# Performance work log

Measured on AMD Instinct MI355X. Metric: run time of the kernel, lower is better.

The kernel has to match this reference:

```python
import jax, jax.numpy as jnp
import numpy as np

B, T, P, H = 64, 64, 32, 256  # batch, seq_len, num_series, hidden


def setup_inputs() -> dict:
    key = jax.random.key(0)
    ks = jax.random.split(key, 16)
    s = 0.05  # weight init scale (keeps gates unsaturated, like PyTorch's 1/sqrt(H) init)
    return {
        'X': jax.random.normal(ks[0], (B, T, P), dtype=jnp.float32),
        'eps': jax.random.normal(ks[1], (1, B, H), dtype=jnp.float32),
        'W_ih_enc': jax.random.normal(ks[2], (3 * H, P), dtype=jnp.float32) * s,
        'W_hh_enc': jax.random.normal(ks[3], (3 * H, H), dtype=jnp.float32) * s,
        'b_ih_enc': jax.random.normal(ks[4], (3 * H,), dtype=jnp.float32) * s,
        'b_hh_enc': jax.random.normal(ks[5], (3 * H,), dtype=jnp.float32) * s,
        'fc_mu_w': jax.random.normal(ks[6], (H, H), dtype=jnp.float32) * s,
        'fc_mu_b': jax.random.normal(ks[7], (H,), dtype=jnp.float32) * s,
        'fc_std_w': jax.random.normal(ks[8], (H, H), dtype=jnp.float32) * s,
        'fc_std_b': jax.random.normal(ks[9], (H,), dtype=jnp.float32) * s,
        'W_ih_dec': jax.random.normal(ks[10], (P, 3 * H, P), dtype=jnp.float32) * s,
        'W_hh_dec': jax.random.normal(ks[11], (P, 3 * H, H), dtype=jnp.float32) * s,
        'b_ih_dec': jax.random.normal(ks[12], (P, 3 * H), dtype=jnp.float32) * s,
        'b_hh_dec': jax.random.normal(ks[13], (P, 3 * H), dtype=jnp.float32) * s,
        'lin_w': jax.random.normal(ks[14], (P, 1, H), dtype=jnp.float32) * s,
        'lin_b': jax.random.normal(ks[15], (P, 1), dtype=jnp.float32) * s,
    }


def _gru_scan(x_seq, h0, Wih, Whh, bih, bhh):
    """PyTorch-convention GRU over x_seq [B,T,in] with h0 [B,H]. Returns (h_last, hs [B,T,H])."""
    Hh = Whh.shape[1]
    # batch the input projection for all timesteps at once
    gi = jnp.einsum('bti,gi->btg', x_seq, Wih) + bih  # [B,T,3H]

    def step(h, gi_t):
        gh = h @ Whh.T + bhh
        r = jax.nn.sigmoid(gi_t[:, :Hh] + gh[:, :Hh])
        zg = jax.nn.sigmoid(gi_t[:, Hh:2 * Hh] + gh[:, Hh:2 * Hh])
        n = jnp.tanh(gi_t[:, 2 * Hh:] + r * gh[:, 2 * Hh:])
        h_new = (1.0 - zg) * n + zg * h
        return h_new, h_new

    h_last, hs = jax.lax.scan(step, h0, jnp.swapaxes(gi, 0, 1))
    return h_last, jnp.swapaxes(hs, 0, 1)


def reference(X, eps, W_ih_enc, W_hh_enc, b_ih_enc, b_hh_enc,
              fc_mu_w, fc_mu_b, fc_std_w, fc_std_b,
              W_ih_dec, W_hh_dec, b_ih_dec, b_hh_dec, lin_w, lin_b):
    # phase=0, mode='train'. Padded Xp = cat(zeros[:, :1], X); Xp[:,1:11] == X[:,0:10].
    Bb = X.shape[0]
    h0 = jnp.zeros((Bb, H), X.dtype)
    h_t, _ = _gru_scan(X[:, 0:10, :], h0, W_ih_enc, W_hh_enc, b_ih_enc, b_hh_enc)  # [B,H]
    mu = h_t @ fc_mu_w.T + fc_mu_b
    log_var = h_t @ fc_std_w.T + fc_std_b
    sigma = jnp.exp(0.5 * log_var)
    z = mu + sigma * eps[0]  # reparameterization; eps plays the role of torch.randn

    # decoder input: cat(Xp[:,0:1], Xp[:,11:-1]) == cat(zeros step, X[:,10:T-1])  -> [B, T-10, P]
    dec_in = jnp.concatenate([jnp.zeros_like(X[:, :1, :]), X[:, 10:-1, :]], axis=1)

    def one_series(Wih, Whh, bih, bhh, lw, lb):
        _, hs = _gru_scan(dec_in, z, Wih, Whh, bih, bhh)  # [B, T-10, H]
        return jnp.einsum('bth,oh->bto', hs, lw) + lb     # [B, T-10, 1]

    # connection is all-ones -> every decoder sees the full dec_in; vmap over stacked params
    pred = jax.vmap(one_series)(W_ih_dec, W_hh_dec, b_ih_dec, b_hh_dec, lin_w, lin_b)  # [P,B,T-10,1]
    return pred, log_var[None], mu[None]
```

## Files before the change

kernel.cpp:

```cpp
#include <hip/hip_runtime.h>

typedef unsigned int u32;
typedef unsigned short u16;
typedef __attribute__((ext_vector_type(8))) short short8;
typedef __attribute__((ext_vector_type(4))) float f32x4;

#define DEV static __device__ __forceinline__

DEV float b2f(u16 v){ union{u32 u; float f;} c; c.u = ((u32)v) << 16; return c.f; }
DEV u16 f2b(float f){ union{float ff; u32 u;} c; c.ff = f; return (u16)((c.u + 0x7fffu + ((c.u >> 16) & 1u)) >> 16); }
DEV float sigm(float x){ return 1.f/(1.f + __expf(-x)); }
DEV float tanh_(float x){ float e = __expf(-2.f*x); return (1.f-e)/(1.f+e); }

#define SER_STRIDE 221184

#define BLDS_U16 (48*3*64*8)
#define HXA_U16  (8*64*8)
#define XA_U16   (2*64*8)
#define LWF_U16  (8*5*8)
#define SMEM_BYTES ((BLDS_U16 + HXA_U16 + XA_U16 + LWF_U16)*2)

DEV int hxi(int m, int c){ return (((c>>5)<<6) + m + (((c>>3)&3)<<4))*8 + (c&7); }

__global__ __launch_bounds__(64) void pack_kernel(
    const float* __restrict__ WihD, const float* __restrict__ WhhD,
    const float* __restrict__ WihE, const float* __restrict__ WhhE,
    u16* __restrict__ wsB)
{
  const int ps = blockIdx.y;
  const int f  = blockIdx.x;
  const int n0 = f / 9, k = f - n0*9;
  const int lane = threadIdx.x;
  const int n = lane & 15, q = lane >> 4;
  const int row = n0*16 + n;
  const float* Whh = (ps < 32) ? WhhD + ps*196608 : WhhE;
  const float* Wih = (ps < 32) ? WihD + ps*24576  : WihE;
  const float* src = (k < 8) ? (Whh + row*256 + k*32 + q*8) : (Wih + row*32 + q*8);
  u32 wd[4];
  #pragma unroll
  for (int j = 0; j < 4; ++j) {
    u16 lo = f2b(src[2*j]);
    u16 hi = f2b(src[2*j+1]);
    wd[j] = (u32)lo | ((u32)hi << 16);
  }
  uint4* dst = (uint4*)(wsB + (((size_t)ps*432 + f)*64 + lane)*8);
  *dst = make_uint4(wd[0], wd[1], wd[2], wd[3]);
}

template<int NSTEPS, bool IS_DEC>
DEV void gru_body(u16* hxA, u16* xA, u16* Blds, u16* lwfc,
                  const u16* __restrict__ Bp,
                  const float* __restrict__ bihP, const float* __restrict__ bhhP,
                  const float* __restrict__ X, const float* __restrict__ z0,
                  const float* __restrict__ lwp, const float* __restrict__ lbp,
                  float* __restrict__ predp, int b0)
{
  const int tid = threadIdx.x;
  const int w = tid >> 6, lane = tid & 63;
  const int n = lane & 15, q = lane >> 4;

  for (int idx = tid; idx < (HXA_U16 + XA_U16)/2; idx += 512)
    ((u32*)hxA)[idx] = 0;
  __syncthreads();

  if (IS_DEC) {
    const int m = tid >> 6, c0 = (tid*4) & 255;
    float4 v = *(const float4*)&z0[(b0+m)*256 + c0];
    const int base = hxi(m, c0);
    hxA[base]   = f2b(v.x); hxA[base+1] = f2b(v.y);
    hxA[base+2] = f2b(v.z); hxA[base+3] = f2b(v.w);
  } else {
    if (tid < 256) {
      const int m = tid >> 5, c = tid & 31;
      xA[(m + 16*(c>>3))*8 + (c&7)] = f2b(X[(b0+m)*2048 + c]);
    }
  }

  if (IS_DEC && tid < 320) {
    const int k0 = tid / 40, rem = tid - k0*40;
    const int r = rem >> 3, j = rem & 7;
    lwfc[(k0*5 + r)*8 + j] = (r < 4) ? f2b(lwp[k0*32 + r*8 + j]) : (u16)0;
  }

  #pragma unroll
  for (int r = 0; r < 18; ++r) {
    const int g = r*512 + tid;
    const int frag = g >> 6, e = g & 63;
    const int nt = frag / 3, kk = frag - nt*3;
    ((uint4*)Blds)[g] = ((const uint4*)Bp)[((size_t)nt*9 + 6 + kk)*64 + e];
  }

  short8 Bres[36];
  #pragma unroll
  for (int i = 0; i < 2; ++i)
    #pragma unroll
    for (int g = 0; g < 3; ++g)
      #pragma unroll
      for (int k = 0; k < 6; ++k)
        Bres[(i*3+g)*6 + k] =
          *(const short8*)(Bp + (((size_t)(g*16 + 2*w + i)*9 + k)*64 + lane)*8);
  #pragma unroll
  for (int r = 0; r < 36; ++r)
    asm volatile("" : "+v"(Bres[r]));

  float br[2], bz[2], bnx[2], bnh[2];
  #pragma unroll
  for (int i = 0; i < 2; ++i) {
    const int col = (2*w + i)*16 + n;
    br[i]  = bihP[col]     + bhhP[col];
    bz[i]  = bihP[256+col] + bhhP[256+col];
    bnx[i] = bihP[512+col];
    bnh[i] = bhhP[512+col];
  }
  const float lb = IS_DEC ? lbp[0] : 0.f;
  __syncthreads();

  #pragma unroll 1
  for (int t = 0; t < NSTEPS; ++t) {
    short8 af[9];
    #pragma unroll
    for (int k0 = 0; k0 < 8; ++k0)
      af[k0] = *(const short8*)&hxA[(k0*64 + lane)*8];
    af[8] = *(const short8*)&xA[(t&1)*512 + lane*8];

    if (IS_DEC && w == 0 && t > 0) {
      f32x4 lp = {0,0,0,0};
      #pragma unroll
      for (int k0 = 0; k0 < 8; ++k0) {
        const short8 lf = *(const short8*)&lwfc[(k0*5 + ((n==0) ? q : 4))*8];
        lp = __builtin_amdgcn_mfma_f32_16x16x32_bf16(af[k0], lf, lp, 0,0,0);
      }
      if (n == 0 && q < 2) {
        #pragma unroll
        for (int rr = 0; rr < 4; ++rr)
          predp[(b0 + q*4 + rr)*54 + (t-1)] = lp[rr] + lb;
      }
    }

    if (t+1 < NSTEPS && tid < 256) {
      const int m = tid >> 5, c = tid & 31;
      const float v = X[(b0+m)*2048 + ((IS_DEC ? (t+10) : (t+1)))*32 + c];
      xA[((t+1)&1)*512 + (m + 16*(c>>3))*8 + (c&7)] = f2b(v);
    }

    float hnew[2][4];
    #pragma unroll
    for (int i = 0; i < 2; ++i) {
      const int ntr =  0 + 2*w + i, ntz = 16 + 2*w + i, ntn = 32 + 2*w + i;
      f32x4 ar={0,0,0,0}, az={0,0,0,0}, anh={0,0,0,0}, anx={0,0,0,0};
      {
        short8 b6 = *(const short8*)&Blds[((ntr*3+0)*64+lane)*8];
        short8 b7 = *(const short8*)&Blds[((ntr*3+1)*64+lane)*8];
        short8 b8 = *(const short8*)&Blds[((ntr*3+2)*64+lane)*8];
        #pragma unroll
        for (int k = 0; k < 6; ++k)
          ar = __builtin_amdgcn_mfma_f32_16x16x32_bf16(af[k], Bres[(i*3+0)*6+k], ar, 0,0,0);
        ar = __builtin_amdgcn_mfma_f32_16x16x32_bf16(af[6], b6, ar, 0,0,0);
        ar = __builtin_amdgcn_mfma_f32_16x16x32_bf16(af[7], b7, ar, 0,0,0);
        ar = __builtin_amdgcn_mfma_f32_16x16x32_bf16(af[8], b8, ar, 0,0,0);
      }
      {
        short8 b6 = *(const short8*)&Blds[((ntz*3+0)*64+lane)*8];
        short8 b7 = *(const short8*)&Blds[((ntz*3+1)*64+lane)*8];
        short8 b8 = *(const short8*)&Blds[((ntz*3+2)*64+lane)*8];
        #pragma unroll
        for (int k = 0; k < 6; ++k)
          az = __builtin_amdgcn_mfma_f32_16x16x32_bf16(af[k], Bres[(i*3+1)*6+k], az, 0,0,0);
        az = __builtin_amdgcn_mfma_f32_16x16x32_bf16(af[6], b6, az, 0,0,0);
        az = __builtin_amdgcn_mfma_f32_16x16x32_bf16(af[7], b7, az, 0,0,0);
        az = __builtin_amdgcn_mfma_f32_16x16x32_bf16(af[8], b8, az, 0,0,0);
      }
      {
        short8 b6 = *(const short8*)&Blds[((ntn*3+0)*64+lane)*8];
        short8 b7 = *(const short8*)&Blds[((ntn*3+1)*64+lane)*8];
        short8 b8 = *(const short8*)&Blds[((ntn*3+2)*64+lane)*8];
        #pragma unroll
        for (int k = 0; k < 6; ++k)
          anh = __builtin_amdgcn_mfma_f32_16x16x32_bf16(af[k], Bres[(i*3+2)*6+k], anh, 0,0,0);
        anh = __builtin_amdgcn_mfma_f32_16x16x32_bf16(af[6], b6, anh, 0,0,0);
        anh = __builtin_amdgcn_mfma_f32_16x16x32_bf16(af[7], b7, anh, 0,0,0);
        anx = __builtin_amdgcn_mfma_f32_16x16x32_bf16(af[8], b8, anx, 0,0,0);
      }
      const int col = (2*w + i)*16 + n;
      #pragma unroll
      for (int rr = 0; rr < 4; ++rr) {
        const int m = q*4 + rr;
        const float rg = sigm(ar[rr] + br[i]);
        const float zg = sigm(az[rr] + bz[i]);
        const float nv = tanh_(anx[rr] + bnx[i] + rg*(anh[rr] + bnh[i]));
        const float hold = b2f(hxA[hxi(m, col)]);
        hnew[i][rr] = (1.f - zg)*nv + zg*hold;
      }
    }
    __syncthreads();
    if (q < 2) {
      #pragma unroll
      for (int i = 0; i < 2; ++i) {
        const int col = (2*w + i)*16 + n;
        #pragma unroll
        for (int rr = 0; rr < 4; ++rr)
          hxA[hxi(q*4 + rr, col)] = f2b(hnew[i][rr]);
      }
    }
    __syncthreads();
  }

  if (IS_DEC && w == 0) {
    short8 afx[8];
    #pragma unroll
    for (int k0 = 0; k0 < 8; ++k0)
      afx[k0] = *(const short8*)&hxA[(k0*64 + lane)*8];
    f32x4 lp = {0,0,0,0};
    #pragma unroll
    for (int k0 = 0; k0 < 8; ++k0) {
      const short8 lf = *(const short8*)&lwfc[(k0*5 + ((n==0) ? q : 4))*8];
      lp = __builtin_amdgcn_mfma_f32_16x16x32_bf16(afx[k0], lf, lp, 0,0,0);
    }
    if (n == 0 && q < 2) {
      #pragma unroll
      for (int rr = 0; rr < 4; ++rr)
        predp[(b0 + q*4 + rr)*54 + (NSTEPS-1)] = lp[rr] + lb;
    }
  }
}

__global__ __launch_bounds__(512, 2) void enc_lat(
    const u16* __restrict__ wsB,
    const float* __restrict__ bih, const float* __restrict__ bhh,
    const float* __restrict__ X,
    const float* __restrict__ Wmu, const float* __restrict__ bmu,
    const float* __restrict__ Wsd, const float* __restrict__ bsd,
    const float* __restrict__ eps,
    float* __restrict__ z, float* __restrict__ out_lv, float* __restrict__ out_mu)
{
  extern __shared__ char smem[];
  u16* Blds = (u16*)smem;
  u16* hxA  = Blds + BLDS_U16;
  u16* xA   = hxA + HXA_U16;
  u16* lwfc = xA + XA_U16;
  const int b0 = blockIdx.y * 8;
  gru_body<10, false>(hxA, xA, Blds, lwfc, wsB + (size_t)32*SER_STRIDE,
                      bih, bhh, X, nullptr, nullptr, nullptr, nullptr, b0);
  __syncthreads();
  const int tid = threadIdx.x;
  const int j = tid & 255, half = tid >> 8;
  float am[4] = {0,0,0,0}, as[4] = {0,0,0,0};
  const float* wmrow = Wmu + j*256;
  const float* wsrow = Wsd + j*256;
  #pragma unroll 2
  for (int c0 = 0; c0 < 256; c0 += 8) {
    float4 wm0 = *(const float4*)&wmrow[c0];
    float4 wm1 = *(const float4*)&wmrow[c0+4];
    float4 ws0 = *(const float4*)&wsrow[c0];
    float4 ws1 = *(const float4*)&wsrow[c0+4];
    #pragma unroll
    for (int mm = 0; mm < 4; ++mm) {
      const u16* hp = &hxA[hxi(half*4 + mm, c0)];
      float h0x=b2f(hp[0]), h0y=b2f(hp[1]), h0z=b2f(hp[2]), h0w=b2f(hp[3]);
      float h1x=b2f(hp[4]), h1y=b2f(hp[5]), h1z=b2f(hp[6]), h1w=b2f(hp[7]);
      am[mm] += wm0.x*h0x + wm0.y*h0y + wm0.z*h0z + wm0.w*h0w
              + wm1.x*h1x + wm1.y*h1y + wm1.z*h1z + wm1.w*h1w;
      as[mm] += ws0.x*h0x + ws0.y*h0y + ws0.z*h0z + ws0.w*h0w
              + ws1.x*h1x + ws1.y*h1y + ws1.z*h1z + ws1.w*h1w;
    }
  }
  #pragma unroll
  for (int mm = 0; mm < 4; ++mm) {
    const int b = b0 + half*4 + mm;
    const float mu = am[mm] + bmu[j];
    const float lv = as[mm] + bsd[j];
    const float zv = mu + __expf(0.5f*lv) * eps[b*256 + j];
    z[b*256 + j]      = zv;
    out_lv[b*256 + j] = lv;
    out_mu[b*256 + j] = mu;
  }
}

__global__ __launch_bounds__(512, 2) void dec_mfma(
    const u16* __restrict__ wsB,
    const float* __restrict__ bih, const float* __restrict__ bhh,
    const float* __restrict__ X, const float* __restrict__ z,
    const float* __restrict__ lin_w, const float* __restrict__ lin_b,
    float* __restrict__ pred)
{
  extern __shared__ char smem[];
  u16* Blds = (u16*)smem;
  u16* hxA  = Blds + BLDS_U16;
  u16* xA   = hxA + HXA_U16;
  u16* lwfc = xA + XA_U16;
  const int p = blockIdx.x;
  const int b0 = blockIdx.y * 8;
  gru_body<54, true>(hxA, xA, Blds, lwfc, wsB + (size_t)p*SER_STRIDE,
                     bih + p*768, bhh + p*768, X, z,
                     lin_w + p*256, lin_b + p, pred + p*3456, b0);
}

extern "C" void kernel_launch(void* const* d_in, const int* in_sizes, int n_in,
                              void* d_out, int out_size, void* d_ws, size_t ws_size,
                              hipStream_t stream) {
  const float* X        = (const float*)d_in[0];
  const float* eps      = (const float*)d_in[1];
  const float* Wih_enc  = (const float*)d_in[2];
  const float* Whh_enc  = (const float*)d_in[3];
  const float* bih_enc  = (const float*)d_in[4];
  const float* bhh_enc  = (const float*)d_in[5];
  const float* fc_mu_w  = (const float*)d_in[6];
  const float* fc_mu_b  = (const float*)d_in[7];
  const float* fc_std_w = (const float*)d_in[8];
  const float* fc_std_b = (const float*)d_in[9];
  const float* Wih_dec  = (const float*)d_in[10];
  const float* Whh_dec  = (const float*)d_in[11];
  const float* bih_dec  = (const float*)d_in[12];
  const float* bhh_dec  = (const float*)d_in[13];
  const float* lin_w    = (const float*)d_in[14];
  const float* lin_b    = (const float*)d_in[15];

  float* out    = (float*)d_out;
  float* pred   = out;
  float* out_lv = out + 110592;
  float* out_mu = out + 126976;

  u16*   wsB = (u16*)d_ws;
  float* z   = (float*)((char*)d_ws + (size_t)33*SER_STRIDE*2);

  (void)hipFuncSetAttribute((const void*)enc_lat,
      hipFuncAttributeMaxDynamicSharedMemorySize, SMEM_BYTES);
  (void)hipFuncSetAttribute((const void*)dec_mfma,
      hipFuncAttributeMaxDynamicSharedMemorySize, SMEM_BYTES);

  pack_kernel<<<dim3(432, 33), 64, 0, stream>>>(Wih_dec, Whh_dec, Wih_enc, Whh_enc, wsB);
  enc_lat<<<dim3(1, 8), 512, SMEM_BYTES, stream>>>(
      wsB, bih_enc, bhh_enc, X,
      fc_mu_w, fc_mu_b, fc_std_w, fc_std_b, eps, z, out_lv, out_mu);
  dec_mfma<<<dim3(32, 8), 512, SMEM_BYTES, stream>>>(
      wsB, bih_dec, bhh_dec, X, z, lin_w, lin_b, pred);
}
```

Baseline: 327.6 us.

## Double-buffer hidden state to drop a barrier and split gate epilogue across lanes

The hidden state now lives in a ping-pong LDS buffer with a compact 8-row A layout, so each step needs one __syncthreads instead of two. The old state is carried in registers instead of being reloaded from LDS. Gate nonlinearities are split across all four lane groups via a shuffle, so every lane does half the epilogue work instead of only half the lanes storing. The X prefetch load is issued early, MFMA chains for the three gates are interleaved for ILP, and the pack kernel uses 256-thread blocks. Risks include extra shuffles and layout mistakes in the new A-fragment indexing.

```diff
diff --git a/kernel.cpp b/kernel.cpp
--- a/kernel.cpp
+++ b/kernel.cpp
@@ -15,22 +15,22 @@
 #define SER_STRIDE 221184
 
 #define BLDS_U16 (48*3*64*8)
-#define HXA_U16  (8*64*8)
-#define XA_U16   (2*64*8)
-#define LWF_U16  (8*5*8)
-#define SMEM_BYTES ((BLDS_U16 + HXA_U16 + XA_U16 + LWF_U16)*2)
-
-DEV int hxi(int m, int c){ return (((c>>5)<<6) + m + (((c>>3)&3)<<4))*8 + (c&7); }
-
-__global__ __launch_bounds__(64) void pack_kernel(
+#define HA_U16   (2*2048)
+#define XAB_U16  (2*256)
+#define LWF_U16  256
+#define SMEM_BYTES ((BLDS_U16 + HA_U16 + XAB_U16 + LWF_U16)*2)
+
+DEV int hxi(int m, int c){ return (((c>>5)*32) + (((c>>3)&3)*8) + m)*8 + (c&7); }
+
+__global__ __launch_bounds__(256) void pack_kernel(
     const float* __restrict__ WihD, const float* __restrict__ WhhD,
     const float* __restrict__ WihE, const float* __restrict__ WhhE,
     u16* __restrict__ wsB)
 {
   const int ps = blockIdx.y;
-  const int f  = blockIdx.x;
+  const int f  = blockIdx.x*4 + (threadIdx.x >> 6);
   const int n0 = f / 9, k = f - n0*9;
-  const int lane = threadIdx.x;
+  const int lane = threadIdx.x & 63;
   const int n = lane & 15, q = lane >> 4;
   const int row = n0*16 + n;
   const float* Whh = (ps < 32) ? WhhD + ps*196608 : WhhE;
@@ -43,12 +43,11 @@
     u16 hi = f2b(src[2*j+1]);
     wd[j] = (u32)lo | ((u32)hi << 16);
   }
-  uint4* dst = (uint4*)(wsB + (((size_t)ps*432 + f)*64 + lane)*8);
-  *dst = make_uint4(wd[0], wd[1], wd[2], wd[3]);
+  *(uint4*)(wsB + (((size_t)ps*432 + f)*64 + lane)*8) = make_uint4(wd[0], wd[1], wd[2], wd[3]);
 }
 
 template<int NSTEPS, bool IS_DEC>
-DEV void gru_body(u16* hxA, u16* xA, u16* Blds, u16* lwfc,
+DEV void gru_body(u16* hA, u16* xA, u16* Blds, u16* lwfc,
                   const u16* __restrict__ Bp,
                   const float* __restrict__ bihP, const float* __restrict__ bhhP,
                   const float* __restrict__ X, const float* __restrict__ z0,
@@ -58,29 +57,26 @@
   const int tid = threadIdx.x;
   const int w = tid >> 6, lane = tid & 63;
   const int n = lane & 15, q = lane >> 4;
-
-  for (int idx = tid; idx < (HXA_U16 + XA_U16)/2; idx += 512)
-    ((u32*)hxA)[idx] = 0;
+  const int isel  = q >> 1;
+  const int mbase = (q & 1) * 4;
+  const int colS  = (2*w + isel)*16 + n;
+
+  for (int idx = tid; idx < (HA_U16 + XAB_U16)/2; idx += 512)
+    ((u32*)hA)[idx] = 0;
   __syncthreads();
 
   if (IS_DEC) {
     const int m = tid >> 6, c0 = (tid*4) & 255;
     float4 v = *(const float4*)&z0[(b0+m)*256 + c0];
     const int base = hxi(m, c0);
-    hxA[base]   = f2b(v.x); hxA[base+1] = f2b(v.y);
-    hxA[base+2] = f2b(v.z); hxA[base+3] = f2b(v.w);
-  } else {
-    if (tid < 256) {
-      const int m = tid >> 5, c = tid & 31;
-      xA[(m + 16*(c>>3))*8 + (c&7)] = f2b(X[(b0+m)*2048 + c]);
-    }
-  }
-
-  if (IS_DEC && tid < 320) {
-    const int k0 = tid / 40, rem = tid - k0*40;
-    const int r = rem >> 3, j = rem & 7;
-    lwfc[(k0*5 + r)*8 + j] = (r < 4) ? f2b(lwp[k0*32 + r*8 + j]) : (u16)0;
-  }
+    hA[base]   = f2b(v.x); hA[base+1] = f2b(v.y);
+    hA[base+2] = f2b(v.z); hA[base+3] = f2b(v.w);
+  } else if (tid < 256) {
+    const int m = tid >> 5, c = tid & 31;
+    xA[((c>>3)*8 + m)*8 + (c&7)] = f2b(X[(b0+m)*2048 + c]);
+  }
+  if (IS_DEC && tid < 256)
+    lwfc[tid] = f2b(lwp[tid]);
 
   #pragma unroll
   for (int r = 0; r < 18; ++r) {
@@ -103,31 +99,41 @@
   for (int r = 0; r < 36; ++r)
     asm volatile("" : "+v"(Bres[r]));
 
-  float br[2], bz[2], bnx[2], bnh[2];
-  #pragma unroll
-  for (int i = 0; i < 2; ++i) {
-    const int col = (2*w + i)*16 + n;
-    br[i]  = bihP[col]     + bhhP[col];
-    bz[i]  = bihP[256+col] + bhhP[256+col];
-    bnx[i] = bihP[512+col];
-    bnh[i] = bhhP[512+col];
-  }
+  const float brS  = bihP[colS]     + bhhP[colS];
+  const float bzS  = bihP[256+colS] + bhhP[256+colS];
+  const float bnxS = bihP[512+colS];
+  const float bnhS = bhhP[512+colS];
   const float lb = IS_DEC ? lbp[0] : 0.f;
+
+  float hold[4];
+  #pragma unroll
+  for (int rr = 0; rr < 4; ++rr)
+    hold[rr] = IS_DEC ? b2f(f2b(z0[(b0 + mbase + rr)*256 + colS])) : 0.f;
+
+  const int wbase = hxi(mbase, colS);
   __syncthreads();
 
   #pragma unroll 1
   for (int t = 0; t < NSTEPS; ++t) {
+    const int par = t & 1;
+    u16* hP = hA + par*2048;
+
+    float xv = 0.f;
+    const bool doX = (t+1 < NSTEPS) && (tid < 256);
+    const int xm = tid >> 5, xc = tid & 31;
+    if (doX) xv = X[(b0+xm)*2048 + (IS_DEC ? (t+10) : (t+1))*32 + xc];
+
     short8 af[9];
     #pragma unroll
     for (int k0 = 0; k0 < 8; ++k0)
-      af[k0] = *(const short8*)&hxA[(k0*64 + lane)*8];
-    af[8] = *(const short8*)&xA[(t&1)*512 + lane*8];
+      af[k0] = *(const short8*)&hP[(k0*32 + q*8 + (n&7))*8];
+    af[8] = *(const short8*)&xA[par*256 + (q*8 + (n&7))*8];
 
     if (IS_DEC && w == 0 && t > 0) {
       f32x4 lp = {0,0,0,0};
       #pragma unroll
       for (int k0 = 0; k0 < 8; ++k0) {
-        const short8 lf = *(const short8*)&lwfc[(k0*5 + ((n==0) ? q : 4))*8];
+        const short8 lf = *(const short8*)&lwfc[(k0*4 + q)*8];
         lp = __builtin_amdgcn_mfma_f32_16x16x32_bf16(af[k0], lf, lp, 0,0,0);
       }
       if (n == 0 && q < 2) {
@@ -137,84 +143,70 @@
       }
     }
 
-    if (t+1 < NSTEPS && tid < 256) {
-      const int m = tid >> 5, c = tid & 31;
-      const float v = X[(b0+m)*2048 + ((IS_DEC ? (t+10) : (t+1)))*32 + c];
-      xA[((t+1)&1)*512 + (m + 16*(c>>3))*8 + (c&7)] = f2b(v);
-    }
-
-    float hnew[2][4];
+    if (doX) xA[(par^1)*256 + ((xc>>3)*8 + xm)*8 + (xc&7)] = f2b(xv);
+
+    f32x4 accr[2], accz[2], accnh[2], accnx[2];
     #pragma unroll
     for (int i = 0; i < 2; ++i) {
-      const int ntr =  0 + 2*w + i, ntz = 16 + 2*w + i, ntn = 32 + 2*w + i;
+      const int ntr = 2*w + i, ntz = 16 + 2*w + i, ntn = 32 + 2*w + i;
       f32x4 ar={0,0,0,0}, az={0,0,0,0}, anh={0,0,0,0}, anx={0,0,0,0};
-      {
-        short8 b6 = *(const short8*)&Blds[((ntr*3+0)*64+lane)*8];
-        short8 b7 = *(const short8*)&Blds[((ntr*3+1)*64+lane)*8];
-        short8 b8 = *(const short8*)&Blds[((ntr*3+2)*64+lane)*8];
-        #pragma unroll
-        for (int k = 0; k < 6; ++k)
-          ar = __builtin_amdgcn_mfma_f32_16x16x32_bf16(af[k], Bres[(i*3+0)*6+k], ar, 0,0,0);
-        ar = __builtin_amdgcn_mfma_f32_16x16x32_bf16(af[6], b6, ar, 0,0,0);
-        ar = __builtin_amdgcn_mfma_f32_16x16x32_bf16(af[7], b7, ar, 0,0,0);
-        ar = __builtin_amdgcn_mfma_f32_16x16x32_bf16(af[8], b8, ar, 0,0,0);
+      const short8 b6r = *(const short8*)&Blds[((ntr*3+0)*64+lane)*8];
+      const short8 b7r = *(const short8*)&Blds[((ntr*3+1)*64+lane)*8];
+      const short8 b8r = *(const short8*)&Blds[((ntr*3+2)*64+lane)*8];
+      const short8 b6z = *(const short8*)&Blds[((ntz*3+0)*64+lane)*8];
+      const short8 b7z = *(const short8*)&Blds[((ntz*3+1)*64+lane)*8];
+      const short8 b8z = *(const short8*)&Blds[((ntz*3+2)*64+lane)*8];
+      const short8 b6n = *(const short8*)&Blds[((ntn*3+0)*64+lane)*8];
+      const short8 b7n = *(const short8*)&Blds[((ntn*3+1)*64+lane)*8];
+      const short8 b8n = *(const short8*)&Blds[((ntn*3+2)*64+lane)*8];
+      #pragma unroll
+      for (int k = 0; k < 6; ++k) {
+        ar  = __builtin_amdgcn_mfma_f32_16x16x32_bf16(af[k], Bres[(i*3+0)*6+k], ar, 0,0,0);
+        az  = __builtin_amdgcn_mfma_f32_16x16x32_bf16(af[k], Bres[(i*3+1)*6+k], az, 0,0,0);
+        anh = __builtin_amdgcn_mfma_f32_16x16x32_bf16(af[k], Bres[(i*3+2)*6+k], anh, 0,0,0);
       }
-      {
-        short8 b6 = *(const short8*)&Blds[((ntz*3+0)*64+lane)*8];
-        short8 b7 = *(const short8*)&Blds[((ntz*3+1)*64+lane)*8];
-        short8 b8 = *(const short8*)&Blds[((ntz*3+2)*64+lane)*8];
-        #pragma unroll
-        for (int k = 0; k < 6; ++k)
-          az = __builtin_amdgcn_mfma_f32_16x16x32_bf16(af[k], Bres[(i*3+1)*6+k], az, 0,0,0);
-        az = __builtin_amdgcn_mfma_f32_16x16x32_bf16(af[6], b6, az, 0,0,0);
-        az = __builtin_amdgcn_mfma_f32_16x16x32_bf16(af[7], b7, az, 0,0,0);
-        az = __builtin_amdgcn_mfma_f32_16x16x32_bf16(af[8], b8, az, 0,0,0);
-      }
-      {
-        short8 b6 = *(const short8*)&Blds[((ntn*3+0)*64+lane)*8];
-        short8 b7 = *(const short8*)&Blds[((ntn*3+1)*64+lane)*8];
-        short8 b8 = *(const short8*)&Blds[((ntn*3+2)*64+lane)*8];
-        #pragma unroll
-        for (int k = 0; k < 6; ++k)
-          anh = __builtin_amdgcn_mfma_f32_16x16x32_bf16(af[k], Bres[(i*3+2)*6+k], anh, 0,0,0);
-        anh = __builtin_amdgcn_mfma_f32_16x16x32_bf16(af[6], b6, anh, 0,0,0);
-        anh = __builtin_amdgcn_mfma_f32_16x16x32_bf16(af[7], b7, anh, 0,0,0);
-        anx = __builtin_amdgcn_mfma_f32_16x16x32_bf16(af[8], b8, anx, 0,0,0);
-      }
-      const int col = (2*w + i)*16 + n;
-      #pragma unroll
-      for (int rr = 0; rr < 4; ++rr) {
-        const int m = q*4 + rr;
-        const float rg = sigm(ar[rr] + br[i]);
-        const float zg = sigm(az[rr] + bz[i]);
-        const float nv = tanh_(anx[rr] + bnx[i] + rg*(anh[rr] + bnh[i]));
-        const float hold = b2f(hxA[hxi(m, col)]);
-        hnew[i][rr] = (1.f - zg)*nv + zg*hold;
-      }
+      ar  = __builtin_amdgcn_mfma_f32_16x16x32_bf16(af[6], b6r, ar, 0,0,0);
+      ar  = __builtin_amdgcn_mfma_f32_16x16x32_bf16(af[7], b7r, ar, 0,0,0);
+      ar  = __builtin_amdgcn_mfma_f32_16x16x32_bf16(af[8], b8r, ar, 0,0,0);
+      az  = __builtin_amdgcn_mfma_f32_16x16x32_bf16(af[6], b6z, az, 0,0,0);
+      az  = __builtin_amdgcn_mfma_f32_16x16x32_bf16(af[7], b7z, az, 0,0,0);
+      az  = __builtin_amdgcn_mfma_f32_16x16x32_bf16(af[8], b8z, az, 0,0,0);
+      anh = __builtin_amdgcn_mfma_f32_16x16x32_bf16(af[6], b6n, anh, 0,0,0);
+      anh = __builtin_amdgcn_mfma_f32_16x16x32_bf16(af[7], b7n, anh, 0,0,0);
+      anx = __builtin_amdgcn_mfma_f32_16x16x32_bf16(af[8], b8n, anx, 0,0,0);
+      accr[i] = ar; accz[i] = az; accnh[i] = anh; accnx[i] = anx;
+    }
+
+    u16* hW = hA + (par^1)*2048;
+    #pragma unroll
+    for (int rr = 0; rr < 4; ++rr) {
+      const float r1  = __shfl_xor(accr[1][rr],  32, 64);
+      const float z1  = __shfl_xor(accz[1][rr],  32, 64);
+      const float nh1 = __shfl_xor(accnh[1][rr], 32, 64);
+      const float nx1 = __shfl_xor(accnx[1][rr], 32, 64);
+      const float arv  = (q >= 2) ? r1  : accr[0][rr];
+      const float azv  = (q >= 2) ? z1  : accz[0][rr];
+      const float anhv = (q >= 2) ? nh1 : accnh[0][rr];
+      const float anxv = (q >= 2) ? nx1 : accnx[0][rr];
+      const float rg = sigm(arv + brS);
+      const float zg = sigm(azv + bzS);
+      const float nv = tanh_(anxv + bnxS + rg*(anhv + bnhS));
+      const float hn = (1.f - zg)*nv + zg*hold[rr];
+      const u16 hb = f2b(hn);
+      hold[rr] = b2f(hb);
+      hW[wbase + rr*8] = hb;
     }
     __syncthreads();
-    if (q < 2) {
-      #pragma unroll
-      for (int i = 0; i < 2; ++i) {
-        const int col = (2*w + i)*16 + n;
-        #pragma unroll
-        for (int rr = 0; rr < 4; ++rr)
-          hxA[hxi(q*4 + rr, col)] = f2b(hnew[i][rr]);
-      }
-    }
-    __syncthreads();
   }
 
   if (IS_DEC && w == 0) {
-    short8 afx[8];
-    #pragma unroll
-    for (int k0 = 0; k0 < 8; ++k0)
-      afx[k0] = *(const short8*)&hxA[(k0*64 + lane)*8];
+    const u16* hF = hA + (NSTEPS&1)*2048;
     f32x4 lp = {0,0,0,0};
     #pragma unroll
     for (int k0 = 0; k0 < 8; ++k0) {
-      const short8 lf = *(const short8*)&lwfc[(k0*5 + ((n==0) ? q : 4))*8];
-      lp = __builtin_amdgcn_mfma_f32_16x16x32_bf16(afx[k0], lf, lp, 0,0,0);
+      const short8 a = *(const short8*)&hF[(k0*32 + q*8 + (n&7))*8];
+      const short8 lf = *(const short8*)&lwfc[(k0*4 + q)*8];
+      lp = __builtin_amdgcn_mfma_f32_16x16x32_bf16(a, lf, lp, 0,0,0);
     }
     if (n == 0 && q < 2) {
       #pragma unroll
@@ -235,11 +227,11 @@
 {
   extern __shared__ char smem[];
   u16* Blds = (u16*)smem;
-  u16* hxA  = Blds + BLDS_U16;
-  u16* xA   = hxA + HXA_U16;
-  u16* lwfc = xA + XA_U16;
+  u16* hA   = Blds + BLDS_U16;
+  u16* xA   = hA + HA_U16;
+  u16* lwfc = xA + XAB_U16;
   const int b0 = blockIdx.y * 8;
-  gru_body<10, false>(hxA, xA, Blds, lwfc, wsB + (size_t)32*SER_STRIDE,
+  gru_body<10, false>(hA, xA, Blds, lwfc, wsB + (size_t)32*SER_STRIDE,
                       bih, bhh, X, nullptr, nullptr, nullptr, nullptr, b0);
   __syncthreads();
   const int tid = threadIdx.x;
@@ -247,6 +239,7 @@
   float am[4] = {0,0,0,0}, as[4] = {0,0,0,0};
   const float* wmrow = Wmu + j*256;
   const float* wsrow = Wsd + j*256;
+  const u16* hF = hA + ((10)&1)*2048;
   #pragma unroll 2
   for (int c0 = 0; c0 < 256; c0 += 8) {
     float4 wm0 = *(const float4*)&wmrow[c0];
@@ -255,7 +248,7 @@
     float4 ws1 = *(const float4*)&wsrow[c0+4];
     #pragma unroll
     for (int mm = 0; mm < 4; ++mm) {
-      const u16* hp = &hxA[hxi(half*4 + mm, c0)];
+      const u16* hp = &hF[hxi(half*4 + mm, c0)];
       float h0x=b2f(hp[0]), h0y=b2f(hp[1]), h0z=b2f(hp[2]), h0w=b2f(hp[3]);
       float h1x=b2f(hp[4]), h1y=b2f(hp[5]), h1z=b2f(hp[6]), h1w=b2f(hp[7]);
       am[mm] += wm0.x*h0x + wm0.y*h0y + wm0.z*h0z + wm0.w*h0w
@@ -285,12 +278,12 @@
 {
   extern __shared__ char smem[];
   u16* Blds = (u16*)smem;
-  u16* hxA  = Blds + BLDS_U16;
-  u16* xA   = hxA + HXA_U16;
-  u16* lwfc = xA + XA_U16;
+  u16* hA   = Blds + BLDS_U16;
+  u16* xA   = hA + HA_U16;
+  u16* lwfc = xA + XAB_U16;
   const int p = blockIdx.x;
   const int b0 = blockIdx.y * 8;
-  gru_body<54, true>(hxA, xA, Blds, lwfc, wsB + (size_t)p*SER_STRIDE,
+  gru_body<54, true>(hA, xA, Blds, lwfc, wsB + (size_t)p*SER_STRIDE,
                      bih + p*768, bhh + p*768, X, z,
                      lin_w + p*256, lin_b + p, pred + p*3456, b0);
 }
@@ -328,7 +321,7 @@
   (void)hipFuncSetAttribute((const void*)dec_mfma,
       hipFuncAttributeMaxDynamicSharedMemorySize, SMEM_BYTES);
 
-  pack_kernel<<<dim3(432, 33), 64, 0, stream>>>(Wih_dec, Whh_dec, Wih_enc, Whh_enc, wsB);
+  pack_kernel<<<dim3(108, 33), 256, 0, stream>>>(Wih_dec, Whh_dec, Wih_enc, Whh_enc, wsB);
   enc_lat<<<dim3(1, 8), 512, SMEM_BYTES, stream>>>(
       wsB, bih_enc, bhh_enc, X,
       fc_mu_w, fc_mu_b, fc_std_w, fc_std_b, eps, z, out_lv, out_mu);
```

New measurement: 280.4 us. 14.4% less time.
